# Kernel tuning notes

Measured on AMD Instinct MI355X. Metric: run time of the kernel, lower is better.

The kernel has to match this reference:

```python
import jax, jax.numpy as jnp
import numpy as np

N = 10000
E = 320000
F_IN = 256
HID = 256
C_OUT = 40
NUM_BASES = 10
NUM_REL = 2


def _rgcn_layer(x, edge_index, edge_type, basis, comp, root, bias):
    # basis: [B, d_in, d_out], comp: [R, B] -> per-relation weights [R, d_in, d_out]
    W = jnp.einsum('rb,bio->rio', comp, basis)
    src, dst = edge_index[0], edge_index[1]
    n = x.shape[0]
    out = x @ root + bias  # self/root transform
    xg = x[src]  # [E, d_in] gathered source features
    for r in range(NUM_REL):  # fixed small relation count
        m = (edge_type == r).astype(x.dtype)  # [E]
        msg = (xg @ W[r]) * m[:, None]  # [E, d_out]
        s = jax.ops.segment_sum(msg, dst, num_segments=n)
        cnt = jax.ops.segment_sum(m, dst, num_segments=n)
        out = out + s / jnp.maximum(cnt, 1.0)[:, None]  # mean aggregation (PyG RGCNConv default)
    return out


def setup_inputs() -> dict:
    key = jax.random.key(0)
    ks = jax.random.split(key, 16)
    inp = {
        'x': jax.random.normal(ks[0], (N, F_IN), dtype=jnp.float32),
        'edge_index': jax.random.randint(ks[1], (2, E), 0, N, dtype=jnp.int64),
        'edge_type': jax.random.randint(ks[2], (E,), 0, NUM_REL, dtype=jnp.int64),
    }
    dims = [(F_IN, HID), (HID, HID), (HID, C_OUT)]
    for i, (di, do) in enumerate(dims, start=1):
        s = 1.0 / np.sqrt(di)
        inp[f'basis{i}'] = jax.random.normal(ks[3 * i], (NUM_BASES, di, do), dtype=jnp.float32) * s
        inp[f'comp{i}'] = jax.random.normal(ks[3 * i + 1], (NUM_REL, NUM_BASES), dtype=jnp.float32)
        inp[f'root{i}'] = jax.random.normal(ks[3 * i + 2], (di, do), dtype=jnp.float32) * s
        inp[f'bias{i}'] = jnp.zeros((do,), dtype=jnp.float32)
    return inp


def reference(x, edge_index, edge_type,
              basis1, comp1, root1, bias1,
              basis2, comp2, root2, bias2,
              basis3, comp3, root3, bias3):
    # layer 1 + relu (dropout is identity in eval mode)
    x = _rgcn_layer(x, edge_index, edge_type, basis1, comp1, root1, bias1)
    x = jax.nn.relu(x)
    # layer 2 + relu
    x = _rgcn_layer(x, edge_index, edge_type, basis2, comp2, root2, bias2)
    x = jax.nn.relu(x)
    # final layer + log_softmax over classes
    x = _rgcn_layer(x, edge_index, edge_type, basis3, comp3, root3, bias3)
    return jax.nn.log_softmax(x, axis=1)
```

## Files before the change

kernel.cpp:

```cpp
#include <hip/hip_runtime.h>
#include <math.h>

#define NREL 2
#define NB 10
#define C_OUT 40
#define CAP 64

typedef unsigned int u32;
typedef unsigned short u16;
typedef __attribute__((ext_vector_type(8))) short bf16x8;
typedef __attribute__((ext_vector_type(4))) float f32x4;

#define MFMA16 __builtin_amdgcn_mfma_f32_16x16x32_bf16

__device__ __forceinline__ u32 pack_split(float v) {
    u32 u = __float_as_uint(v);
    u32 hi = (u + 0x7FFFu + ((u >> 16) & 1u)) & 0xFFFF0000u;
    float r = v - __uint_as_float(hi);
    u32 ur = __float_as_uint(r);
    u32 lo = ((ur + 0x7FFFu + ((ur >> 16) & 1u)) >> 16) & 0xFFFFu;
    return hi | lo;
}
__device__ __forceinline__ float bfbits(u32 w) { return __uint_as_float(w); }

__global__ void fused_pre(const float* __restrict__ x, u16* __restrict__ xP,
                          int* __restrict__ cnt, int M2, int n2) {
    int g = blockIdx.x * 256 + threadIdx.x;
    if (g < M2) cnt[g] = 0;
    if (g >= n2) return;
    int i = g * 2;
    int row = i >> 8, f = i & 255;
    u32 p0 = pack_split(x[i]);
    u32 p1 = pack_split(x[i + 1]);
    *(u32*)&xP[(size_t)row * 512 + f] = (p0 >> 16) | (p1 & 0xFFFF0000u);
    *(u32*)&xP[(size_t)row * 512 + 256 + f] = (p0 & 0xFFFFu) | (p1 << 16);
}

__global__ void fill_edges_cap(const int* __restrict__ ei, const int* __restrict__ et,
                               int* __restrict__ cnt, int* __restrict__ elist, int E_) {
    int e = blockIdx.x * 256 + threadIdx.x;
    if (e < E_) {
        int src = ei[e];
        int dst = ei[E_ + e];
        int r = et[e];
        int idx = dst * 2 + r;
        int pos = atomicAdd(&cnt[idx], 1);
        if (pos < CAP) elist[idx * CAP + pos] = src;
    }
}

__global__ void build_wt_all(const float* __restrict__ basis1, const float* __restrict__ comp1,
                             const float* __restrict__ root1, u16* __restrict__ Wt1,
                             const float* __restrict__ basis2, const float* __restrict__ comp2,
                             const float* __restrict__ root2, u16* __restrict__ Wt2,
                             const float* __restrict__ basis3, const float* __restrict__ comp3,
                             const float* __restrict__ root3, u16* __restrict__ Wt3) {
    int layer = blockIdx.y;
    const float* basis = (layer == 0) ? basis1 : (layer == 1) ? basis2 : basis3;
    const float* comp = (layer == 0) ? comp1 : (layer == 1) ? comp2 : comp3;
    const float* root = (layer == 0) ? root1 : (layer == 1) ? root2 : root3;
    u16* Wt = (layer == 0) ? Wt1 : (layer == 1) ? Wt2 : Wt3;
    int dreal = (layer == 2) ? C_OUT : 256;
    int dpad = (layer == 2) ? 64 : 256;

    int c = threadIdx.x;
    if (c >= dpad) return;
    size_t WHS = (size_t)(dpad >> 4) * 24 * 512;
    int k0 = blockIdx.x * 4;
    float cw[NREL][NB];
#pragma unroll
    for (int r = 0; r < NREL; ++r)
#pragma unroll
        for (int b = 0; b < NB; ++b) cw[r][b] = comp[r * NB + b];
#pragma unroll
    for (int t = 0; t < 4; ++t) {
        int k = k0 + t;
        float v = 0.f;
        if (c < dreal) {
            if (k < 256) {
                v = root[k * dreal + c];
            } else {
                int r = (k - 256) >> 8;
                int i = (k - 256) & 255;
#pragma unroll
                for (int b = 0; b < NB; ++b)
                    v += cw[r][b] * basis[(b * 256 + i) * dreal + c];
            }
        }
        u32 pk = pack_split(v);
        int cb = c >> 4, kc = k >> 5, kg = (k >> 3) & 3, e = k & 7;
        size_t idx = ((size_t)(cb * 24 + kc) * 64 + (kg * 16 + (c & 15))) * 8 + e;
        Wt[idx] = (u16)(pk >> 16);
        Wt[WHS + idx] = (u16)(pk & 0xFFFFu);
    }
}

__global__ __launch_bounds__(256) void agg_wave(const u16* __restrict__ hP,
                                                const int* __restrict__ cnt,
                                                const int* __restrict__ elist,
                                                u16* __restrict__ aggP, int M2) {
    int wid = blockIdx.x * 4 + (threadIdx.x >> 6);
    if (wid >= M2) return;
    int lane = threadIdx.x & 63;
    int c = cnt[wid];
    int cc = min(c, CAP);
    const int* ep = elist + (size_t)wid * CAP;
    int myidx = (lane < cc) ? ep[lane] : 0;
    int fo = lane << 2;

    float s0 = 0.f, s1 = 0.f, s2 = 0.f, s3 = 0.f;
    int j = 0;
    for (; j + 3 < cc; j += 4) {
        int e0 = __shfl(myidx, j, 64);
        int e1 = __shfl(myidx, j + 1, 64);
        int e2 = __shfl(myidx, j + 2, 64);
        int e3 = __shfl(myidx, j + 3, 64);
        uint2 h0 = *(const uint2*)(hP + (size_t)e0 * 512 + fo);
        uint2 h1 = *(const uint2*)(hP + (size_t)e1 * 512 + fo);
        uint2 h2 = *(const uint2*)(hP + (size_t)e2 * 512 + fo);
        uint2 h3 = *(const uint2*)(hP + (size_t)e3 * 512 + fo);
        s0 += bfbits(h0.x << 16) + bfbits(h1.x << 16) + bfbits(h2.x << 16) + bfbits(h3.x << 16);
        s1 += bfbits(h0.x & 0xFFFF0000u) + bfbits(h1.x & 0xFFFF0000u) +
              bfbits(h2.x & 0xFFFF0000u) + bfbits(h3.x & 0xFFFF0000u);
        s2 += bfbits(h0.y << 16) + bfbits(h1.y << 16) + bfbits(h2.y << 16) + bfbits(h3.y << 16);
        s3 += bfbits(h0.y & 0xFFFF0000u) + bfbits(h1.y & 0xFFFF0000u) +
              bfbits(h2.y & 0xFFFF0000u) + bfbits(h3.y & 0xFFFF0000u);
    }
    for (; j < cc; ++j) {
        int e0 = __shfl(myidx, j, 64);
        uint2 h0 = *(const uint2*)(hP + (size_t)e0 * 512 + fo);
        s0 += bfbits(h0.x << 16);
        s1 += bfbits(h0.x & 0xFFFF0000u);
        s2 += bfbits(h0.y << 16);
        s3 += bfbits(h0.y & 0xFFFF0000u);
    }

    float inv = (c > 0) ? 1.f / (float)c : 0.f;
    u32 p0 = pack_split(s0 * inv);
    u32 p1 = pack_split(s1 * inv);
    u32 p2 = pack_split(s2 * inv);
    u32 p3 = pack_split(s3 * inv);

    int n = wid >> 1, r = wid & 1;
    u16* orow = aggP + (size_t)n * 1024 + r * 256 + fo;
    uint2 hw, lw;
    hw.x = (p0 >> 16) | (p1 & 0xFFFF0000u);
    hw.y = (p2 >> 16) | (p3 & 0xFFFF0000u);
    lw.x = (p0 & 0xFFFFu) | (p1 << 16);
    lw.y = (p2 & 0xFFFFu) | (p3 << 16);
    *(uint2*)orow = hw;
    *(uint2*)(orow + 512) = lw;
}

__global__ __launch_bounds__(256) void gemm_mfma_big(
    const u16* __restrict__ A0, const u16* __restrict__ A1,
    const u16* __restrict__ Wf, const float* __restrict__ bias,
    u16* __restrict__ OutP, int M) {
    __shared__ u16 ldsA[48 * 512];
    int tid = threadIdx.x;
    int lane = tid & 63;
    int w = tid >> 6;
    int l15 = lane & 15, l4 = lane >> 4;
    int rb0 = blockIdx.x * 16;

    {
        uint4 sv[12];
#pragma unroll
        for (int i = 0; i < 12; ++i) {
            int u = i * 4 + w;
            int p = (u >= 24) ? 1 : 0;
            int kc = u - p * 24;
            const u16* src = (kc < 8)
                ? A0 + (size_t)(rb0 + l15) * 512 + p * 256 + kc * 32 + l4 * 8
                : A1 + (size_t)(rb0 + l15) * 1024 + p * 512 + (kc - 8) * 32 + l4 * 8;
            sv[i] = *(const uint4*)src;
        }
#pragma unroll
        for (int i = 0; i < 12; ++i) {
            int u = i * 4 + w;
            *(uint4*)&ldsA[(size_t)u * 512 + lane * 8] = sv[i];
        }
    }
    __syncthreads();

    const u16* wbase = Wf + (size_t)w * 4 * 24 * 512 + lane * 8;
    f32x4 acc[4] = {};
    bf16x8 pa[4][2], pb[4][4];

    auto LOADC = [&](int c, int s) {
        pa[s][0] = *(const bf16x8*)&ldsA[(size_t)c * 512 + lane * 8];
        pa[s][1] = *(const bf16x8*)&ldsA[(size_t)(24 + c) * 512 + lane * 8];
#pragma unroll
        for (int ct = 0; ct < 4; ++ct)
            pb[s][ct] = *(const bf16x8*)&wbase[(size_t)(ct * 24 + c) * 512];
    };

    LOADC(0, 0);
    LOADC(1, 1);
    LOADC(2, 2);
#pragma unroll
    for (int c = 0; c < 24; ++c) {
        const int s = c & 3;
        if (c + 3 < 24) LOADC(c + 3, (c + 3) & 3);
#pragma unroll
        for (int ct = 0; ct < 4; ++ct) {
            acc[ct] = MFMA16(pa[s][0], pb[s][ct], acc[ct], 0, 0, 0);
            acc[ct] = MFMA16(pa[s][1], pb[s][ct], acc[ct], 0, 0, 0);
        }
    }

#pragma unroll
    for (int ct = 0; ct < 4; ++ct) {
        int col = w * 64 + ct * 16 + l15;
        float b = bias[col];
#pragma unroll
        for (int j = 0; j < 4; ++j) {
            int row = rb0 + l4 * 4 + j;
            if (row < M) {
                float v = fmaxf(acc[ct][j] + b, 0.f);
                u32 pk = pack_split(v);
                OutP[(size_t)row * 512 + col] = (u16)(pk >> 16);
                OutP[(size_t)row * 512 + 256 + col] = (u16)(pk & 0xFFFFu);
            }
        }
    }
}

__global__ __launch_bounds__(256) void gemm_mfma_small(
    const u16* __restrict__ A0, const u16* __restrict__ A1,
    const u16* __restrict__ Wf, const float* __restrict__ bias,
    float* __restrict__ Out, int M) {
    int tid = threadIdx.x;
    int lane = tid & 63;
    int w = tid >> 6;
    int l15 = lane & 15, l4 = lane >> 4;
    int row0 = blockIdx.x * 64 + w * 16;
    int arow = row0 + l15;

    const u16* a0b = A0 + (size_t)arow * 512 + l4 * 8;
    const u16* a1b = A1 + (size_t)arow * 1024 + l4 * 8;
    const u16* wb = Wf + lane * 8;
    const u16* wbl = wb + 4 * 24 * 512;

    f32x4 acc[3] = {};
    bf16x8 pa[2][2], pbh[2][3], pbl[2][3];

    auto LOADC = [&](int c, int s) {
        if (c < 8) {
            pa[s][0] = *(const bf16x8*)(a0b + c * 32);
            pa[s][1] = *(const bf16x8*)(a0b + 256 + c * 32);
        } else {
            pa[s][0] = *(const bf16x8*)(a1b + (c - 8) * 32);
            pa[s][1] = *(const bf16x8*)(a1b + 512 + (c - 8) * 32);
        }
#pragma unroll
        for (int ct = 0; ct < 3; ++ct) {
            pbh[s][ct] = *(const bf16x8*)(wb + (size_t)(ct * 24 + c) * 512);
            pbl[s][ct] = *(const bf16x8*)(wbl + (size_t)(ct * 24 + c) * 512);
        }
    };

    LOADC(0, 0);
#pragma unroll
    for (int c = 0; c < 24; ++c) {
        const int s = c & 1;
        if (c + 1 < 24) LOADC(c + 1, (c + 1) & 1);
#pragma unroll
        for (int ct = 0; ct < 3; ++ct) {
            acc[ct] = MFMA16(pa[s][0], pbh[s][ct], acc[ct], 0, 0, 0);
            acc[ct] = MFMA16(pa[s][0], pbl[s][ct], acc[ct], 0, 0, 0);
            acc[ct] = MFMA16(pa[s][1], pbh[s][ct], acc[ct], 0, 0, 0);
        }
    }

    bool val2 = (l15 < 8);
    float bq0 = bias[l15];
    float bq1 = bias[16 + l15];
    float bq2 = val2 ? bias[32 + l15] : 0.f;

#pragma unroll
    for (int j = 0; j < 4; ++j) {
        float v0 = acc[0][j] + bq0;
        float v1 = acc[1][j] + bq1;
        float v2 = val2 ? (acc[2][j] + bq2) : -INFINITY;
        float m = fmaxf(fmaxf(v0, v1), v2);
#pragma unroll
        for (int d = 1; d < 16; d <<= 1) m = fmaxf(m, __shfl_xor(m, d, 64));
        float s = expf(v0 - m) + expf(v1 - m) + (val2 ? expf(v2 - m) : 0.f);
#pragma unroll
        for (int d = 1; d < 16; d <<= 1) s += __shfl_xor(s, d, 64);
        float ls = m + logf(s);
        int row = row0 + l4 * 4 + j;
        if (row < M) {
            Out[(size_t)row * C_OUT + l15] = v0 - ls;
            Out[(size_t)row * C_OUT + 16 + l15] = v1 - ls;
            if (val2) Out[(size_t)row * C_OUT + 32 + l15] = v2 - ls;
        }
    }
}

extern "C" void kernel_launch(void* const* d_in, const int* in_sizes, int n_in,
                              void* d_out, int out_size, void* d_ws, size_t ws_size,
                              hipStream_t stream) {
    const float* x = (const float*)d_in[0];
    const int* ei = (const int*)d_in[1];
    const int* et = (const int*)d_in[2];
    const float* basis1 = (const float*)d_in[3];
    const float* comp1 = (const float*)d_in[4];
    const float* root1 = (const float*)d_in[5];
    const float* bias1 = (const float*)d_in[6];
    const float* basis2 = (const float*)d_in[7];
    const float* comp2 = (const float*)d_in[8];
    const float* root2 = (const float*)d_in[9];
    const float* bias2 = (const float*)d_in[10];
    const float* basis3 = (const float*)d_in[11];
    const float* comp3 = (const float*)d_in[12];
    const float* root3 = (const float*)d_in[13];
    const float* bias3 = (const float*)d_in[14];

    int N_ = in_sizes[0] / 256;
    int E_ = in_sizes[2];
    int M2 = 2 * N_;
    int Mpad = (N_ + 63) & ~63;

    char* p = (char*)d_ws;
    size_t o = 0;
    auto alloc = [&](size_t bytes) {
        void* r = p + o;
        o += (bytes + 255) & ~(size_t)255;
        return r;
    };
    int* cnt = (int*)alloc((size_t)M2 * 4);
    int* elist = (int*)alloc((size_t)M2 * CAP * 4);
    u16* Wf1 = (u16*)alloc((size_t)2 * 16 * 24 * 512 * 2);
    u16* Wf2 = (u16*)alloc((size_t)2 * 16 * 24 * 512 * 2);
    u16* Wf3 = (u16*)alloc((size_t)2 * 4 * 24 * 512 * 2);
    u16* xP = (u16*)alloc((size_t)Mpad * 512 * 2);
    u16* h1P = (u16*)alloc((size_t)Mpad * 512 * 2);
    u16* aggP = (u16*)alloc((size_t)Mpad * 1024 * 2);
    u16* h2P = xP;
    (void)ws_size;

    int n2 = N_ * 128;

    fused_pre<<<(n2 + 255) / 256, 256, 0, stream>>>(x, xP, cnt, M2, n2);
    {
        dim3 g(192, 3);
        build_wt_all<<<g, 256, 0, stream>>>(basis1, comp1, root1, Wf1,
                                            basis2, comp2, root2, Wf2,
                                            basis3, comp3, root3, Wf3);
    }
    fill_edges_cap<<<(E_ + 255) / 256, 256, 0, stream>>>(ei, et, cnt, elist, E_);

    int gblocks = (N_ + 15) / 16;
    int sblocks = (N_ + 63) / 64;
    int ablocks = (M2 + 3) / 4;

    agg_wave<<<ablocks, 256, 0, stream>>>(xP, cnt, elist, aggP, M2);
    gemm_mfma_big<<<gblocks, 256, 0, stream>>>(xP, aggP, Wf1, bias1, h1P, N_);
    agg_wave<<<ablocks, 256, 0, stream>>>(h1P, cnt, elist, aggP, M2);
    gemm_mfma_big<<<gblocks, 256, 0, stream>>>(h1P, aggP, Wf2, bias2, h2P, N_);
    agg_wave<<<ablocks, 256, 0, stream>>>(h2P, cnt, elist, aggP, M2);
    gemm_mfma_small<<<sblocks, 256, 0, stream>>>(h2P, aggP, Wf3, bias3, (float*)d_out, N_);
}
```

Measured before the change: 153.0 us.

## Drop split-bf16 activations to plain bf16 and retile the big GEMM

Activations and aggregated features are now stored as a single round-to-nearest bf16 instead of a hi/lo bf16 pair, which halves gather traffic and removes one MFMA per step in the GEMMs. The aggregation kernel is reworked so each half-wave gathers a different edge with 16-byte loads, and the two halves are combined with a shuffle. The big GEMM moves to 512-thread blocks covering 32 rows, using 8 waves in a 2x4 layout. The cost is lower accuracy, since the low-order correction terms for activations are gone, which may threaten tolerance across three layers.

```diff
diff --git a/kernel.cpp b/kernel.cpp
--- a/kernel.cpp
+++ b/kernel.cpp
@@ -13,6 +13,10 @@
 
 #define MFMA16 __builtin_amdgcn_mfma_f32_16x16x32_bf16
 
+__device__ __forceinline__ u32 rne16(float v) {
+    u32 u = __float_as_uint(v);
+    return (u + 0x7FFFu + ((u >> 16) & 1u)) >> 16;
+}
 __device__ __forceinline__ u32 pack_split(float v) {
     u32 u = __float_as_uint(v);
     u32 hi = (u + 0x7FFFu + ((u >> 16) & 1u)) & 0xFFFF0000u;
@@ -29,11 +33,8 @@
     if (g < M2) cnt[g] = 0;
     if (g >= n2) return;
     int i = g * 2;
-    int row = i >> 8, f = i & 255;
-    u32 p0 = pack_split(x[i]);
-    u32 p1 = pack_split(x[i + 1]);
-    *(u32*)&xP[(size_t)row * 512 + f] = (p0 >> 16) | (p1 & 0xFFFF0000u);
-    *(u32*)&xP[(size_t)row * 512 + 256 + f] = (p0 & 0xFFFFu) | (p1 << 16);
+    u32 w = rne16(x[i]) | (rne16(x[i + 1]) << 16);
+    *(u32*)&xP[i] = w;
 }
 
 __global__ void fill_edges_cap(const int* __restrict__ ei, const int* __restrict__ et,
@@ -65,7 +66,6 @@
 
     int c = threadIdx.x;
     if (c >= dpad) return;
-    size_t WHS = (size_t)(dpad >> 4) * 24 * 512;
     int k0 = blockIdx.x * 4;
     float cw[NREL][NB];
 #pragma unroll
@@ -91,7 +91,7 @@
         int cb = c >> 4, kc = k >> 5, kg = (k >> 3) & 3, e = k & 7;
         size_t idx = ((size_t)(cb * 24 + kc) * 64 + (kg * 16 + (c & 15))) * 8 + e;
         Wt[idx] = (u16)(pk >> 16);
-        Wt[WHS + idx] = (u16)(pk & 0xFFFFu);
+        if (layer == 2) Wt[(size_t)4 * 24 * 512 + idx] = (u16)(pk & 0xFFFFu);
     }
 }
 
@@ -102,57 +102,79 @@
     int wid = blockIdx.x * 4 + (threadIdx.x >> 6);
     if (wid >= M2) return;
     int lane = threadIdx.x & 63;
+    int half = lane >> 5;
+    int fl = (lane & 31) * 8;
     int c = cnt[wid];
     int cc = min(c, CAP);
     const int* ep = elist + (size_t)wid * CAP;
     int myidx = (lane < cc) ? ep[lane] : 0;
-    int fo = lane << 2;
-
-    float s0 = 0.f, s1 = 0.f, s2 = 0.f, s3 = 0.f;
-    int j = 0;
-    for (; j + 3 < cc; j += 4) {
-        int e0 = __shfl(myidx, j, 64);
-        int e1 = __shfl(myidx, j + 1, 64);
-        int e2 = __shfl(myidx, j + 2, 64);
-        int e3 = __shfl(myidx, j + 3, 64);
-        uint2 h0 = *(const uint2*)(hP + (size_t)e0 * 512 + fo);
-        uint2 h1 = *(const uint2*)(hP + (size_t)e1 * 512 + fo);
-        uint2 h2 = *(const uint2*)(hP + (size_t)e2 * 512 + fo);
-        uint2 h3 = *(const uint2*)(hP + (size_t)e3 * 512 + fo);
-        s0 += bfbits(h0.x << 16) + bfbits(h1.x << 16) + bfbits(h2.x << 16) + bfbits(h3.x << 16);
-        s1 += bfbits(h0.x & 0xFFFF0000u) + bfbits(h1.x & 0xFFFF0000u) +
-              bfbits(h2.x & 0xFFFF0000u) + bfbits(h3.x & 0xFFFF0000u);
-        s2 += bfbits(h0.y << 16) + bfbits(h1.y << 16) + bfbits(h2.y << 16) + bfbits(h3.y << 16);
-        s3 += bfbits(h0.y & 0xFFFF0000u) + bfbits(h1.y & 0xFFFF0000u) +
-              bfbits(h2.y & 0xFFFF0000u) + bfbits(h3.y & 0xFFFF0000u);
-    }
-    for (; j < cc; ++j) {
-        int e0 = __shfl(myidx, j, 64);
-        uint2 h0 = *(const uint2*)(hP + (size_t)e0 * 512 + fo);
-        s0 += bfbits(h0.x << 16);
-        s1 += bfbits(h0.x & 0xFFFF0000u);
-        s2 += bfbits(h0.y << 16);
-        s3 += bfbits(h0.y & 0xFFFF0000u);
-    }
-
-    float inv = (c > 0) ? 1.f / (float)c : 0.f;
-    u32 p0 = pack_split(s0 * inv);
-    u32 p1 = pack_split(s1 * inv);
-    u32 p2 = pack_split(s2 * inv);
-    u32 p3 = pack_split(s3 * inv);
-
-    int n = wid >> 1, r = wid & 1;
-    u16* orow = aggP + (size_t)n * 1024 + r * 256 + fo;
-    uint2 hw, lw;
-    hw.x = (p0 >> 16) | (p1 & 0xFFFF0000u);
-    hw.y = (p2 >> 16) | (p3 & 0xFFFF0000u);
-    lw.x = (p0 & 0xFFFFu) | (p1 << 16);
-    lw.y = (p2 & 0xFFFFu) | (p3 << 16);
-    *(uint2*)orow = hw;
-    *(uint2*)(orow + 512) = lw;
-}
-
-__global__ __launch_bounds__(256) void gemm_mfma_big(
+
+    float s0 = 0.f, s1 = 0.f, s2 = 0.f, s3 = 0.f, s4 = 0.f, s5 = 0.f, s6 = 0.f, s7 = 0.f;
+
+#define ACC8(q)                                    \
+    do {                                           \
+        s0 += bfbits((q).x << 16);                 \
+        s1 += bfbits((q).x & 0xFFFF0000u);         \
+        s2 += bfbits((q).y << 16);                 \
+        s3 += bfbits((q).y & 0xFFFF0000u);         \
+        s4 += bfbits((q).z << 16);                 \
+        s5 += bfbits((q).z & 0xFFFF0000u);         \
+        s6 += bfbits((q).w << 16);                 \
+        s7 += bfbits((q).w & 0xFFFF0000u);         \
+    } while (0)
+
+    int fullpairs = cc >> 1;
+    int jp = 0;
+    for (; jp + 3 < fullpairs; jp += 4) {
+        int e0 = __shfl(myidx, 2 * jp + half, 64);
+        int e1 = __shfl(myidx, 2 * jp + 2 + half, 64);
+        int e2 = __shfl(myidx, 2 * jp + 4 + half, 64);
+        int e3 = __shfl(myidx, 2 * jp + 6 + half, 64);
+        uint4 q0 = *(const uint4*)(hP + (size_t)e0 * 256 + fl);
+        uint4 q1 = *(const uint4*)(hP + (size_t)e1 * 256 + fl);
+        uint4 q2 = *(const uint4*)(hP + (size_t)e2 * 256 + fl);
+        uint4 q3 = *(const uint4*)(hP + (size_t)e3 * 256 + fl);
+        ACC8(q0);
+        ACC8(q1);
+        ACC8(q2);
+        ACC8(q3);
+    }
+    for (; jp < fullpairs; ++jp) {
+        int e0 = __shfl(myidx, 2 * jp + half, 64);
+        uint4 q0 = *(const uint4*)(hP + (size_t)e0 * 256 + fl);
+        ACC8(q0);
+    }
+    if (cc & 1) {
+        int e0 = __shfl(myidx, cc - 1, 64);
+        if (half == 0) {
+            uint4 q0 = *(const uint4*)(hP + (size_t)e0 * 256 + fl);
+            ACC8(q0);
+        }
+    }
+#undef ACC8
+
+    s0 += __shfl_xor(s0, 32, 64);
+    s1 += __shfl_xor(s1, 32, 64);
+    s2 += __shfl_xor(s2, 32, 64);
+    s3 += __shfl_xor(s3, 32, 64);
+    s4 += __shfl_xor(s4, 32, 64);
+    s5 += __shfl_xor(s5, 32, 64);
+    s6 += __shfl_xor(s6, 32, 64);
+    s7 += __shfl_xor(s7, 32, 64);
+
+    if (half == 0) {
+        float inv = (c > 0) ? 1.f / (float)c : 0.f;
+        uint4 o;
+        o.x = rne16(s0 * inv) | (rne16(s1 * inv) << 16);
+        o.y = rne16(s2 * inv) | (rne16(s3 * inv) << 16);
+        o.z = rne16(s4 * inv) | (rne16(s5 * inv) << 16);
+        o.w = rne16(s6 * inv) | (rne16(s7 * inv) << 16);
+        int n = wid >> 1, r = wid & 1;
+        *(uint4*)&aggP[(size_t)n * 512 + r * 256 + fl] = o;
+    }
+}
+
+__global__ __launch_bounds__(512) void gemm_mfma_big(
     const u16* __restrict__ A0, const u16* __restrict__ A1,
     const u16* __restrict__ Wf, const float* __restrict__ bias,
     u16* __restrict__ OutP, int M) {
@@ -160,36 +182,37 @@
     int tid = threadIdx.x;
     int lane = tid & 63;
     int w = tid >> 6;
+    int wr = w >> 2, wc = w & 3;
     int l15 = lane & 15, l4 = lane >> 4;
-    int rb0 = blockIdx.x * 16;
+    int rb0 = blockIdx.x * 32;
 
     {
-        uint4 sv[12];
-#pragma unroll
-        for (int i = 0; i < 12; ++i) {
-            int u = i * 4 + w;
-            int p = (u >= 24) ? 1 : 0;
-            int kc = u - p * 24;
-            const u16* src = (kc < 8)
-                ? A0 + (size_t)(rb0 + l15) * 512 + p * 256 + kc * 32 + l4 * 8
-                : A1 + (size_t)(rb0 + l15) * 1024 + p * 512 + (kc - 8) * 32 + l4 * 8;
+        uint4 sv[6];
+#pragma unroll
+        for (int i = 0; i < 6; ++i) {
+            int u = i * 8 + w;
+            int r16 = (u >= 24) ? 1 : 0;
+            int kc = u - r16 * 24;
+            int row = rb0 + r16 * 16 + l15;
+            const u16* src = (kc < 8) ? A0 + (size_t)row * 256 + kc * 32 + l4 * 8
+                                      : A1 + (size_t)row * 512 + (kc - 8) * 32 + l4 * 8;
             sv[i] = *(const uint4*)src;
         }
 #pragma unroll
-        for (int i = 0; i < 12; ++i) {
-            int u = i * 4 + w;
+        for (int i = 0; i < 6; ++i) {
+            int u = i * 8 + w;
             *(uint4*)&ldsA[(size_t)u * 512 + lane * 8] = sv[i];
         }
     }
     __syncthreads();
 
-    const u16* wbase = Wf + (size_t)w * 4 * 24 * 512 + lane * 8;
+    const u16* wbase = Wf + (size_t)wc * 4 * 24 * 512 + lane * 8;
+    const u16* abase = ldsA + (size_t)wr * 24 * 512 + lane * 8;
     f32x4 acc[4] = {};
-    bf16x8 pa[4][2], pb[4][4];
+    bf16x8 pa[4], pb[4][4];
 
     auto LOADC = [&](int c, int s) {
-        pa[s][0] = *(const bf16x8*)&ldsA[(size_t)c * 512 + lane * 8];
-        pa[s][1] = *(const bf16x8*)&ldsA[(size_t)(24 + c) * 512 + lane * 8];
+        pa[s] = *(const bf16x8*)&abase[(size_t)c * 512];
 #pragma unroll
         for (int ct = 0; ct < 4; ++ct)
             pb[s][ct] = *(const bf16x8*)&wbase[(size_t)(ct * 24 + c) * 512];
@@ -203,24 +226,20 @@
         const int s = c & 3;
         if (c + 3 < 24) LOADC(c + 3, (c + 3) & 3);
 #pragma unroll
-        for (int ct = 0; ct < 4; ++ct) {
-            acc[ct] = MFMA16(pa[s][0], pb[s][ct], acc[ct], 0, 0, 0);
-            acc[ct] = MFMA16(pa[s][1], pb[s][ct], acc[ct], 0, 0, 0);
-        }
+        for (int ct = 0; ct < 4; ++ct)
+            acc[ct] = MFMA16(pa[s], pb[s][ct], acc[ct], 0, 0, 0);
     }
 
 #pragma unroll
     for (int ct = 0; ct < 4; ++ct) {
-        int col = w * 64 + ct * 16 + l15;
+        int col = wc * 64 + ct * 16 + l15;
         float b = bias[col];
 #pragma unroll
         for (int j = 0; j < 4; ++j) {
-            int row = rb0 + l4 * 4 + j;
+            int row = rb0 + wr * 16 + l4 * 4 + j;
             if (row < M) {
                 float v = fmaxf(acc[ct][j] + b, 0.f);
-                u32 pk = pack_split(v);
-                OutP[(size_t)row * 512 + col] = (u16)(pk >> 16);
-                OutP[(size_t)row * 512 + 256 + col] = (u16)(pk & 0xFFFFu);
+                OutP[(size_t)row * 256 + col] = (u16)rne16(v);
             }
         }
     }
@@ -237,22 +256,17 @@
     int row0 = blockIdx.x * 64 + w * 16;
     int arow = row0 + l15;
 
-    const u16* a0b = A0 + (size_t)arow * 512 + l4 * 8;
-    const u16* a1b = A1 + (size_t)arow * 1024 + l4 * 8;
+    const u16* a0b = A0 + (size_t)arow * 256 + l4 * 8;
+    const u16* a1b = A1 + (size_t)arow * 512 + l4 * 8;
     const u16* wb = Wf + lane * 8;
     const u16* wbl = wb + 4 * 24 * 512;
 
     f32x4 acc[3] = {};
-    bf16x8 pa[2][2], pbh[2][3], pbl[2][3];
+    bf16x8 pa[2], pbh[2][3], pbl[2][3];
 
     auto LOADC = [&](int c, int s) {
-        if (c < 8) {
-            pa[s][0] = *(const bf16x8*)(a0b + c * 32);
-            pa[s][1] = *(const bf16x8*)(a0b + 256 + c * 32);
-        } else {
-            pa[s][0] = *(const bf16x8*)(a1b + (c - 8) * 32);
-            pa[s][1] = *(const bf16x8*)(a1b + 512 + (c - 8) * 32);
-        }
+        pa[s] = (c < 8) ? *(const bf16x8*)(a0b + c * 32)
+                        : *(const bf16x8*)(a1b + (c - 8) * 32);
 #pragma unroll
         for (int ct = 0; ct < 3; ++ct) {
             pbh[s][ct] = *(const bf16x8*)(wb + (size_t)(ct * 24 + c) * 512);
@@ -267,9 +281,8 @@
         if (c + 1 < 24) LOADC(c + 1, (c + 1) & 1);
 #pragma unroll
         for (int ct = 0; ct < 3; ++ct) {
-            acc[ct] = MFMA16(pa[s][0], pbh[s][ct], acc[ct], 0, 0, 0);
-            acc[ct] = MFMA16(pa[s][0], pbl[s][ct], acc[ct], 0, 0, 0);
-            acc[ct] = MFMA16(pa[s][1], pbh[s][ct], acc[ct], 0, 0, 0);
+            acc[ct] = MFMA16(pa[s], pbh[s][ct], acc[ct], 0, 0, 0);
+            acc[ct] = MFMA16(pa[s], pbl[s][ct], acc[ct], 0, 0, 0);
         }
     }
 
@@ -332,12 +345,12 @@
     };
     int* cnt = (int*)alloc((size_t)M2 * 4);
     int* elist = (int*)alloc((size_t)M2 * CAP * 4);
-    u16* Wf1 = (u16*)alloc((size_t)2 * 16 * 24 * 512 * 2);
-    u16* Wf2 = (u16*)alloc((size_t)2 * 16 * 24 * 512 * 2);
+    u16* Wf1 = (u16*)alloc((size_t)16 * 24 * 512 * 2);
+    u16* Wf2 = (u16*)alloc((size_t)16 * 24 * 512 * 2);
     u16* Wf3 = (u16*)alloc((size_t)2 * 4 * 24 * 512 * 2);
-    u16* xP = (u16*)alloc((size_t)Mpad * 512 * 2);
-    u16* h1P = (u16*)alloc((size_t)Mpad * 512 * 2);
-    u16* aggP = (u16*)alloc((size_t)Mpad * 1024 * 2);
+    u16* xP = (u16*)alloc((size_t)Mpad * 256 * 2);
+    u16* h1P = (u16*)alloc((size_t)Mpad * 256 * 2);
+    u16* aggP = (u16*)alloc((size_t)Mpad * 512 * 2);
     u16* h2P = xP;
     (void)ws_size;
 
@@ -352,14 +365,14 @@
     }
     fill_edges_cap<<<(E_ + 255) / 256, 256, 0, stream>>>(ei, et, cnt, elist, E_);
 
-    int gblocks = (N_ + 15) / 16;
+    int gblocks = (N_ + 31) / 32;
     int sblocks = (N_ + 63) / 64;
     int ablocks = (M2 + 3) / 4;
 
     agg_wave<<<ablocks, 256, 0, stream>>>(xP, cnt, elist, aggP, M2);
-    gemm_mfma_big<<<gblocks, 256, 0, stream>>>(xP, aggP, Wf1, bias1, h1P, N_);
+    gemm_mfma_big<<<gblocks, 512, 0, stream>>>(xP, aggP, Wf1, bias1, h1P, N_);
     agg_wave<<<ablocks, 256, 0, stream>>>(h1P, cnt, elist, aggP, M2);
-    gemm_mfma_big<<<gblocks, 256, 0, stream>>>(h1P, aggP, Wf2, bias2, h2P, N_);
+    gemm_mfma_big<<<gblocks, 512, 0, stream>>>(h1P, aggP, Wf2, bias2, h2P, N_);
     agg_wave<<<ablocks, 256, 0, stream>>>(h2P, cnt, elist, aggP, M2);
     gemm_mfma_small<<<sblocks, 256, 0, stream>>>(h2P, aggP, Wf3, bias3, (float*)d_out, N_);
 }
```

Result: faster. 137.7 us (-10.0%).
